# Kernel optimization log

Hardware: AMD Instinct MI355X
Metric: run time of the kernel (lower is better)

The kernel has to match this reference:

```python
import jax, jax.numpy as jnp
import numpy as np

N_NODES = 50000
N_EDGES = 800000
D_IN = 64
D_OUT = 64


def setup_inputs() -> dict:
    key = jax.random.key(0)
    k1, k2, k3, k4 = jax.random.split(key, 4)
    x = jax.random.normal(k1, (N_NODES, D_IN), dtype=jnp.float32)
    W = jax.random.normal(k2, (D_IN, D_OUT), dtype=jnp.float32) / np.sqrt(D_IN)
    bias = jnp.zeros((D_OUT,), dtype=jnp.float32)
    # learned per-edge weights (AdaptiveEdgeWeightGNN.edge_attr, initialized from fixed_values)
    edge_weight = jax.random.uniform(k3, (N_EDGES,), dtype=jnp.float32)
    edge_index = jax.random.randint(k4, (2, N_EDGES), 0, N_NODES, dtype=jnp.int64)
    return {"x": x, "W": W, "bias": bias, "edge_weight": edge_weight, "edge_index": edge_index}


def reference(x, W, bias, edge_weight, edge_index):
    # PyG GCNConv forward: gcn_norm (add self-loops, symmetric normalization
    # using the edge weights), linear transform, gather-scale-scatter, + bias.
    N = x.shape[0]
    row = edge_index[0]  # source nodes
    col = edge_index[1]  # target nodes
    loop = jnp.arange(N, dtype=edge_index.dtype)
    row = jnp.concatenate([row, loop])
    col = jnp.concatenate([col, loop])
    ew = jnp.concatenate([edge_weight, jnp.ones((N,), dtype=edge_weight.dtype)])
    # degree from edge weights scattered onto target nodes
    deg = jax.ops.segment_sum(ew, col, num_segments=N)
    deg_inv_sqrt = jnp.where(deg > 0, jax.lax.rsqrt(deg), 0.0)
    norm = deg_inv_sqrt[row] * ew * deg_inv_sqrt[col]  # [E+N]
    xw = x @ W  # [N, D_OUT]
    msgs = xw[row] * norm[:, None]  # gather + scale
    out = jax.ops.segment_sum(msgs, col, num_segments=N)  # scatter-add
    return out + bias
```

## Files before the change

kernel.cpp:

```cpp
#include <hip/hip_runtime.h>

#define N_NODES 50000
#define N_EDGES 800000
#define D 64
#define NCHUNK 64
#define CHUNK_E (N_EDGES / NCHUNK)
#define NRANGE 4
#define RANGE_N 16384
#define NB_NODE 196
#define PLACE_BLOCKS (N_EDGES / 256)
#define FLAGBIT 0x80000000u

typedef int iv4 __attribute__((ext_vector_type(4)));

__device__ __forceinline__ unsigned short f2bf(float f) {
    unsigned int u = __float_as_uint(f);
    u += 0x7FFFu + ((u >> 16) & 1u);
    return (unsigned short)(u >> 16);
}
__device__ __forceinline__ float bf2f(unsigned int s) {
    return __uint_as_float(s << 16);
}

__global__ __launch_bounds__(1024) void k_hist(const int* __restrict__ col,
                                               unsigned short* __restrict__ part,
                                               unsigned short* __restrict__ lrank,
                                               unsigned int* __restrict__ partials) {
    __shared__ unsigned int h[RANGE_N / 2];
    int i = blockIdx.x >> 2;
    int j = blockIdx.x & 3;
    int t = threadIdx.x;
    if (blockIdx.x == 0 && t < 256) partials[t] = 0;
    for (int k = t; k < RANGE_N / 2; k += 1024) h[k] = 0;
    __syncthreads();
    int base = i * CHUNK_E;
    for (int e = base + t; e < base + CHUNK_E; e += 1024) {
        int c = col[e];
        if ((c >> 14) == j) {
            int local = c & (RANGE_N - 1);
            int sh = (local & 1) << 4;
            unsigned int lr = atomicAdd(&h[local >> 1], 1u << sh);
            lrank[e] = (unsigned short)((lr >> sh) & 0xffffu);
        }
    }
    __syncthreads();
    for (int k = t; k < RANGE_N; k += 1024) {
        int n = j * RANGE_N + k;
        if (n < N_NODES)
            part[(size_t)i * N_NODES + n] =
                (unsigned short)((h[k >> 1] >> ((k & 1) << 4)) & 0xffffu);
    }
}

__global__ __launch_bounds__(256) void k_scan(unsigned short* __restrict__ part,
                                              int* __restrict__ start,
                                              unsigned int* __restrict__ partials) {
    __shared__ int s[256];
    __shared__ int red[256];
    int b = blockIdx.x, t = threadIdx.x;
    int n = b * 256 + t;
    unsigned int run = 0;
    if (n < N_NODES) {
        unsigned int vals[NCHUNK];
#pragma unroll
        for (int i = 0; i < NCHUNK; ++i)
            vals[i] = part[(size_t)i * N_NODES + n];
#pragma unroll
        for (int i = 0; i < NCHUNK; ++i) {
            part[(size_t)i * N_NODES + n] = (unsigned short)run;
            run += vals[i];
        }
    }
    int cnt = (n < N_NODES) ? (int)run : 0;
    s[t] = cnt;
    __syncthreads();
    for (int off = 1; off < 256; off <<= 1) {
        int a = (t >= off) ? s[t - off] : 0;
        __syncthreads();
        s[t] += a;
        __syncthreads();
    }
    if (t == 255)
        __hip_atomic_store(&partials[b], (unsigned int)s[255] | FLAGBIT,
                           __ATOMIC_RELEASE, __HIP_MEMORY_SCOPE_AGENT);
    unsigned int pv = 0;
    if (t < b) {
        unsigned int v;
        do {
            v = __hip_atomic_load(&partials[t], __ATOMIC_ACQUIRE, __HIP_MEMORY_SCOPE_AGENT);
        } while (!(v & FLAGBIT));
        pv = v & ~FLAGBIT;
    }
    red[t] = (int)pv;
    __syncthreads();
    for (int off = 128; off > 0; off >>= 1) {
        if (t < off) red[t] += red[t + off];
        __syncthreads();
    }
    int offset = red[0];
    if (n <= N_NODES) start[n] = offset + s[t] - cnt;
}

__global__ __launch_bounds__(256) void k_place(const int* __restrict__ ei,
                                               const float* __restrict__ ew,
                                               const int* __restrict__ start,
                                               const unsigned short* __restrict__ part,
                                               const unsigned short* __restrict__ lrank,
                                               unsigned int* __restrict__ rec) {
    int e = blockIdx.x * 256 + threadIdx.x;
    int c = ei[N_EDGES + e];
    int i = e / CHUNK_E;
    int pos = start[c] + (int)part[(size_t)i * N_NODES + c] + (int)lrank[e];
    rec[pos] = (unsigned int)ei[e] | ((unsigned int)f2bf(ew[e]) << 16);
}

__global__ __launch_bounds__(256, 4) void k_xw(const float* __restrict__ x,
                                               const float* __restrict__ W,
                                               const int* __restrict__ start,
                                               const unsigned int* __restrict__ rec,
                                               float* __restrict__ dis,
                                               unsigned short* __restrict__ xw16) {
    __shared__ float Ws[64 * 64];
    __shared__ float dls[64];
    int t = threadIdx.x;
    int r0 = blockIdx.x * 64;
    for (int i = t; i < 1024; i += 256)
        ((float4*)Ws)[i] = ((const float4*)W)[i];

    {
        int q = t >> 2, l = t & 3;
        int node = r0 + q;
        float s = 0.f;
        if (node < N_NODES) {
            int j0 = start[node], j1 = start[node + 1];
            for (int j = j0 + l; j < j1; j += 4) s += bf2f(rec[j] >> 16);
        }
        s += __shfl_xor(s, 1);
        s += __shfl_xor(s, 2);
        if (l == 0 && node < N_NODES) {
            float dv = rsqrtf(1.0f + s);
            dls[q] = dv;
            dis[node] = dv;
        }
    }
    __syncthreads();

    int cg = t & 15;
    int rg = t >> 4;
    int ra = min(r0 + rg,      N_NODES - 1);
    int rb = min(r0 + rg + 16, N_NODES - 1);
    int rc = min(r0 + rg + 32, N_NODES - 1);
    int rd = min(r0 + rg + 48, N_NODES - 1);
    const float4* x4 = (const float4*)x;

    float4 acc0 = make_float4(0.f, 0.f, 0.f, 0.f);
    float4 acc1 = acc0, acc2 = acc0, acc3 = acc0;

#pragma unroll 1
    for (int k4 = 0; k4 < 16; ++k4) {
        float4 xv0 = x4[ra * 16 + k4];
        float4 xv1 = x4[rb * 16 + k4];
        float4 xv2 = x4[rc * 16 + k4];
        float4 xv3 = x4[rd * 16 + k4];
        float4 w0 = *(const float4*)&Ws[(k4 * 4 + 0) * 64 + cg * 4];
        float4 w1 = *(const float4*)&Ws[(k4 * 4 + 1) * 64 + cg * 4];
        float4 w2 = *(const float4*)&Ws[(k4 * 4 + 2) * 64 + cg * 4];
        float4 w3 = *(const float4*)&Ws[(k4 * 4 + 3) * 64 + cg * 4];
        acc0.x = fmaf(xv0.x, w0.x, acc0.x); acc0.y = fmaf(xv0.x, w0.y, acc0.y);
        acc0.z = fmaf(xv0.x, w0.z, acc0.z); acc0.w = fmaf(xv0.x, w0.w, acc0.w);
        acc0.x = fmaf(xv0.y, w1.x, acc0.x); acc0.y = fmaf(xv0.y, w1.y, acc0.y);
        acc0.z = fmaf(xv0.y, w1.z, acc0.z); acc0.w = fmaf(xv0.y, w1.w, acc0.w);
        acc0.x = fmaf(xv0.z, w2.x, acc0.x); acc0.y = fmaf(xv0.z, w2.y, acc0.y);
        acc0.z = fmaf(xv0.z, w2.z, acc0.z); acc0.w = fmaf(xv0.z, w2.w, acc0.w);
        acc0.x = fmaf(xv0.w, w3.x, acc0.x); acc0.y = fmaf(xv0.w, w3.y, acc0.y);
        acc0.z = fmaf(xv0.w, w3.z, acc0.z); acc0.w = fmaf(xv0.w, w3.w, acc0.w);
        acc1.x = fmaf(xv1.x, w0.x, acc1.x); acc1.y = fmaf(xv1.x, w0.y, acc1.y);
        acc1.z = fmaf(xv1.x, w0.z, acc1.z); acc1.w = fmaf(xv1.x, w0.w, acc1.w);
        acc1.x = fmaf(xv1.y, w1.x, acc1.x); acc1.y = fmaf(xv1.y, w1.y, acc1.y);
        acc1.z = fmaf(xv1.y, w1.z, acc1.z); acc1.w = fmaf(xv1.y, w1.w, acc1.w);
        acc1.x = fmaf(xv1.z, w2.x, acc1.x); acc1.y = fmaf(xv1.z, w2.y, acc1.y);
        acc1.z = fmaf(xv1.z, w2.z, acc1.z); acc1.w = fmaf(xv1.z, w2.w, acc1.w);
        acc1.x = fmaf(xv1.w, w3.x, acc1.x); acc1.y = fmaf(xv1.w, w3.y, acc1.y);
        acc1.z = fmaf(xv1.w, w3.z, acc1.z); acc1.w = fmaf(xv1.w, w3.w, acc1.w);
        acc2.x = fmaf(xv2.x, w0.x, acc2.x); acc2.y = fmaf(xv2.x, w0.y, acc2.y);
        acc2.z = fmaf(xv2.x, w0.z, acc2.z); acc2.w = fmaf(xv2.x, w0.w, acc2.w);
        acc2.x = fmaf(xv2.y, w1.x, acc2.x); acc2.y = fmaf(xv2.y, w1.y, acc2.y);
        acc2.z = fmaf(xv2.y, w1.z, acc2.z); acc2.w = fmaf(xv2.y, w1.w, acc2.w);
        acc2.x = fmaf(xv2.z, w2.x, acc2.x); acc2.y = fmaf(xv2.z, w2.y, acc2.y);
        acc2.z = fmaf(xv2.z, w2.z, acc2.z); acc2.w = fmaf(xv2.z, w2.w, acc2.w);
        acc2.x = fmaf(xv2.w, w3.x, acc2.x); acc2.y = fmaf(xv2.w, w3.y, acc2.y);
        acc2.z = fmaf(xv2.w, w3.z, acc2.z); acc2.w = fmaf(xv2.w, w3.w, acc2.w);
        acc3.x = fmaf(xv3.x, w0.x, acc3.x); acc3.y = fmaf(xv3.x, w0.y, acc3.y);
        acc3.z = fmaf(xv3.x, w0.z, acc3.z); acc3.w = fmaf(xv3.x, w0.w, acc3.w);
        acc3.x = fmaf(xv3.y, w1.x, acc3.x); acc3.y = fmaf(xv3.y, w1.y, acc3.y);
        acc3.z = fmaf(xv3.y, w1.z, acc3.z); acc3.w = fmaf(xv3.y, w1.w, acc3.w);
        acc3.x = fmaf(xv3.z, w2.x, acc3.x); acc3.y = fmaf(xv3.z, w2.y, acc3.y);
        acc3.z = fmaf(xv3.z, w2.z, acc3.z); acc3.w = fmaf(xv3.z, w2.w, acc3.w);
        acc3.x = fmaf(xv3.w, w3.x, acc3.x); acc3.y = fmaf(xv3.w, w3.y, acc3.y);
        acc3.z = fmaf(xv3.w, w3.z, acc3.z); acc3.w = fmaf(xv3.w, w3.w, acc3.w);
    }

    float4 accs[4] = { acc0, acc1, acc2, acc3 };
#pragma unroll
    for (int i = 0; i < 4; ++i) {
        int row = r0 + rg + 16 * i;
        if (row < N_NODES) {
            float s = dls[rg + 16 * i];
            ushort4 s4 = make_ushort4(f2bf(accs[i].x * s), f2bf(accs[i].y * s),
                                      f2bf(accs[i].z * s), f2bf(accs[i].w * s));
            *(ushort4*)&xw16[row * 64 + cg * 4] = s4;
        }
    }
}

__global__ __launch_bounds__(256) void k_gather(const int* __restrict__ start,
                                                const unsigned int* __restrict__ rec,
                                                const unsigned short* __restrict__ xw16,
                                                const float* __restrict__ dis,
                                                const float* __restrict__ bias,
                                                float* __restrict__ out) {
    int wave = threadIdx.x >> 6;
    int c = threadIdx.x & 63;
    int n = blockIdx.x * 4 + wave;
    float di = dis[n];
    float acc[8];
#pragma unroll
    for (int k = 0; k < 8; ++k) acc[k] = 0.f;
    acc[0] = bf2f((unsigned int)xw16[n * 64 + c]);
    int j0  = __builtin_amdgcn_readfirstlane(start[n]);
    int cnt = __builtin_amdgcn_readfirstlane(start[n + 1]) - j0;
    int nit = (cnt + 7) >> 3;
    const iv4* rq = (const iv4*)(rec + j0);
    for (int it = 0; it < nit; ++it) {
        iv4 qa = rq[2 * it], qb = rq[2 * it + 1];
        unsigned int r[8];
        r[0] = (unsigned int)__builtin_amdgcn_readfirstlane(qa.x);
        r[1] = (unsigned int)__builtin_amdgcn_readfirstlane(qa.y);
        r[2] = (unsigned int)__builtin_amdgcn_readfirstlane(qa.z);
        r[3] = (unsigned int)__builtin_amdgcn_readfirstlane(qa.w);
        r[4] = (unsigned int)__builtin_amdgcn_readfirstlane(qb.x);
        r[5] = (unsigned int)__builtin_amdgcn_readfirstlane(qb.y);
        r[6] = (unsigned int)__builtin_amdgcn_readfirstlane(qb.z);
        r[7] = (unsigned int)__builtin_amdgcn_readfirstlane(qb.w);
        float v[8];
#pragma unroll
        for (int k = 0; k < 8; ++k)
            v[k] = bf2f((unsigned int)xw16[(r[k] & 0xffffu) * 64 + c]);
        int rem = cnt - (it << 3);
#pragma unroll
        for (int k = 0; k < 8; ++k) {
            float w = (k < rem) ? bf2f(r[k] >> 16) : 0.0f;
            acc[k] = fmaf(v[k], w, acc[k]);
        }
    }
    float a = ((acc[0] + acc[1]) + (acc[2] + acc[3])) + ((acc[4] + acc[5]) + (acc[6] + acc[7]));
    out[n * 64 + c] = fmaf(a, di, bias[c]);
}

extern "C" void kernel_launch(void* const* d_in, const int* in_sizes, int n_in,
                              void* d_out, int out_size, void* d_ws, size_t ws_size,
                              hipStream_t stream) {
    const float* x    = (const float*)d_in[0];
    const float* W    = (const float*)d_in[1];
    const float* bias = (const float*)d_in[2];
    const float* ew   = (const float*)d_in[3];
    const int*   ei   = (const int*)d_in[4];
    float* out = (float*)d_out;

    char* wsb = (char*)d_ws;
    unsigned int*   rec   = (unsigned int*)wsb;
    unsigned short* xw16  = (unsigned short*)(wsb + 6200000);
    unsigned short* lrank = (unsigned short*)(wsb + 12600000);
    unsigned short* part  = (unsigned short*)(wsb + 14200000);
    float*          dis   = (float*)(wsb + 20600000);
    int*            start = (int*)(wsb + 21000000);
    unsigned int*   partials = (unsigned int*)(wsb + 21300000);

    k_hist<<<NCHUNK * NRANGE, 1024, 0, stream>>>(ei + N_EDGES, part, lrank, partials);
    k_scan<<<NB_NODE, 256, 0, stream>>>(part, start, partials);
    k_place<<<PLACE_BLOCKS, 256, 0, stream>>>(ei, ew, start, part, lrank, rec);
    k_xw<<<(N_NODES + 63) / 64, 256, 0, stream>>>(x, W, start, rec, dis, xw16);
    k_gather<<<N_NODES / 4, 256, 0, stream>>>(start, rec, xw16, dis, bias, out);
}
```

Baseline: 84.72 us.

## Split per-node chunk scan across four lanes and launch more scan blocks

The scan kernel now assigns each node to four threads. Each thread handles 16 of the 64 chunk counts, and the four threads combine their sums with a sub-wavefront shuffle scan. Each block covers 64 nodes, so 782 blocks are launched instead of 196. This exposes more memory-level parallelism and occupancy on a kernel that was latency bound with few blocks and 64 serial loads per thread. The trade-off is more blocks in the decoupled-lookback chain: each block now sums up to 781 predecessor flags in a strided loop, which adds spin-wait and global atomic traffic. The partials array is also cleared over 1024 entries.

Result: slower. 157.9 us (+86.4%).

```diff
diff --git a/kernel.cpp b/kernel.cpp
--- a/kernel.cpp
+++ b/kernel.cpp
@@ -7,7 +7,7 @@
 #define CHUNK_E (N_EDGES / NCHUNK)
 #define NRANGE 4
 #define RANGE_N 16384
-#define NB_NODE 196
+#define SCAN_BLOCKS 782
 #define PLACE_BLOCKS (N_EDGES / 256)
 #define FLAGBIT 0x80000000u
 
@@ -30,7 +30,7 @@
     int i = blockIdx.x >> 2;
     int j = blockIdx.x & 3;
     int t = threadIdx.x;
-    if (blockIdx.x == 0 && t < 256) partials[t] = 0;
+    if (blockIdx.x == 0 && t < 1024) partials[t] = 0;
     for (int k = t; k < RANGE_N / 2; k += 1024) h[k] = 0;
     __syncthreads();
     int base = i * CHUNK_E;
@@ -52,53 +52,66 @@
     }
 }
 
-__global__ __launch_bounds__(256) void k_scan(unsigned short* __restrict__ part,
-                                              int* __restrict__ start,
-                                              unsigned int* __restrict__ partials) {
-    __shared__ int s[256];
-    __shared__ int red[256];
+__global__ __launch_bounds__(256, 6) void k_scan(unsigned short* __restrict__ part,
+                                                 int* __restrict__ start,
+                                                 unsigned int* __restrict__ partials) {
+    __shared__ int snode[64];
+    __shared__ int sred[256];
     int b = blockIdx.x, t = threadIdx.x;
-    int n = b * 256 + t;
-    unsigned int run = 0;
+    int q = t >> 2, l = t & 3;
+    int n = b * 64 + q;
+    unsigned int vals[16];
+    unsigned int lsum = 0;
     if (n < N_NODES) {
-        unsigned int vals[NCHUNK];
-#pragma unroll
-        for (int i = 0; i < NCHUNK; ++i)
-            vals[i] = part[(size_t)i * N_NODES + n];
-#pragma unroll
-        for (int i = 0; i < NCHUNK; ++i) {
-            part[(size_t)i * N_NODES + n] = (unsigned short)run;
+#pragma unroll
+        for (int i = 0; i < 16; ++i) {
+            vals[i] = part[(size_t)(l * 16 + i) * N_NODES + n];
+            lsum += vals[i];
+        }
+    }
+    unsigned int x = lsum;
+    unsigned int y = __shfl_up(x, 1, 4); if (l >= 1) x += y;
+    y = __shfl_up(x, 2, 4); if (l >= 2) x += y;
+    unsigned int excl = x - lsum;
+    unsigned int cnt = __shfl(x, 3, 4);
+    if (n < N_NODES) {
+        unsigned int run = excl;
+#pragma unroll
+        for (int i = 0; i < 16; ++i) {
+            part[(size_t)(l * 16 + i) * N_NODES + n] = (unsigned short)run;
             run += vals[i];
         }
     }
-    int cnt = (n < N_NODES) ? (int)run : 0;
-    s[t] = cnt;
-    __syncthreads();
-    for (int off = 1; off < 256; off <<= 1) {
-        int a = (t >= off) ? s[t - off] : 0;
-        __syncthreads();
-        s[t] += a;
-        __syncthreads();
-    }
-    if (t == 255)
-        __hip_atomic_store(&partials[b], (unsigned int)s[255] | FLAGBIT,
-                           __ATOMIC_RELEASE, __HIP_MEMORY_SCOPE_AGENT);
-    unsigned int pv = 0;
-    if (t < b) {
+    if (l == 0) snode[q] = (n < N_NODES) ? (int)cnt : 0;
+    __syncthreads();
+    if (t < 64) {
+        int v = snode[t];
+        int ix = v;
+        for (int off = 1; off < 64; off <<= 1) {
+            int u = __shfl_up(ix, off, 64);
+            if (t >= off) ix += u;
+        }
+        snode[t] = ix - v;
+        if (t == 63)
+            __hip_atomic_store(&partials[b], (unsigned int)ix | FLAGBIT,
+                               __ATOMIC_RELEASE, __HIP_MEMORY_SCOPE_AGENT);
+    }
+    int psum = 0;
+    for (int t2 = t; t2 < b; t2 += 256) {
         unsigned int v;
         do {
-            v = __hip_atomic_load(&partials[t], __ATOMIC_ACQUIRE, __HIP_MEMORY_SCOPE_AGENT);
+            v = __hip_atomic_load(&partials[t2], __ATOMIC_ACQUIRE, __HIP_MEMORY_SCOPE_AGENT);
         } while (!(v & FLAGBIT));
-        pv = v & ~FLAGBIT;
-    }
-    red[t] = (int)pv;
+        psum += (int)(v & ~FLAGBIT);
+    }
+    sred[t] = psum;
     __syncthreads();
     for (int off = 128; off > 0; off >>= 1) {
-        if (t < off) red[t] += red[t + off];
+        if (t < off) sred[t] += sred[t + off];
         __syncthreads();
     }
-    int offset = red[0];
-    if (n <= N_NODES) start[n] = offset + s[t] - cnt;
+    int offset = sred[0];
+    if (l == 0 && n <= N_NODES) start[n] = offset + snode[q];
 }
 
 __global__ __launch_bounds__(256) void k_place(const int* __restrict__ ei,
@@ -277,7 +290,7 @@
     unsigned int*   partials = (unsigned int*)(wsb + 21300000);
 
     k_hist<<<NCHUNK * NRANGE, 1024, 0, stream>>>(ei + N_EDGES, part, lrank, partials);
-    k_scan<<<NB_NODE, 256, 0, stream>>>(part, start, partials);
+    k_scan<<<SCAN_BLOCKS, 256, 0, stream>>>(part, start, partials);
     k_place<<<PLACE_BLOCKS, 256, 0, stream>>>(ei, ew, start, part, lrank, rec);
     k_xw<<<(N_NODES + 63) / 64, 256, 0, stream>>>(x, W, start, rec, dis, xw16);
     k_gather<<<N_NODES / 4, 256, 0, stream>>>(start, rec, xw16, dis, bias, out);
```

## Split node scan into three kernels and parallelize per-node chunk scan across four lanes

Applied to the files above, without the earlier changes.

Replaces the single scan kernel, which had each thread serially read and rewrite 64 chunk counts and used a decoupled look-back spin on flagged partials, with three kernels. The first spreads each node's 64 chunk counts over 4 lanes with a shuffle scan across 782 blocks for more memory parallelism. The second does the block-local scan and writes partials, and the third adds the cross-block prefix. This removes the spin-wait and raises occupancy, at the cost of two extra kernel launches and an extra pass over start.

Result: faster. 82.03 us (median of 2 runs) (-3.2%).

```diff
diff --git a/kernel.cpp b/kernel.cpp
--- a/kernel.cpp
+++ b/kernel.cpp
@@ -7,9 +7,9 @@
 #define CHUNK_E (N_EDGES / NCHUNK)
 #define NRANGE 4
 #define RANGE_N 16384
+#define SCANA_BLOCKS 782
 #define NB_NODE 196
 #define PLACE_BLOCKS (N_EDGES / 256)
-#define FLAGBIT 0x80000000u
 
 typedef int iv4 __attribute__((ext_vector_type(4)));
 
@@ -24,13 +24,11 @@
 
 __global__ __launch_bounds__(1024) void k_hist(const int* __restrict__ col,
                                                unsigned short* __restrict__ part,
-                                               unsigned short* __restrict__ lrank,
-                                               unsigned int* __restrict__ partials) {
+                                               unsigned short* __restrict__ lrank) {
     __shared__ unsigned int h[RANGE_N / 2];
     int i = blockIdx.x >> 2;
     int j = blockIdx.x & 3;
     int t = threadIdx.x;
-    if (blockIdx.x == 0 && t < 256) partials[t] = 0;
     for (int k = t; k < RANGE_N / 2; k += 1024) h[k] = 0;
     __syncthreads();
     int base = i * CHUNK_E;
@@ -52,26 +50,39 @@
     }
 }
 
-__global__ __launch_bounds__(256) void k_scan(unsigned short* __restrict__ part,
-                                              int* __restrict__ start,
-                                              unsigned int* __restrict__ partials) {
+__global__ __launch_bounds__(256) void k_scanA(unsigned short* __restrict__ part,
+                                               int* __restrict__ nodecnt) {
+    int b = blockIdx.x, t = threadIdx.x;
+    int q = t >> 2, l = t & 3;
+    int n = b * 64 + q;
+    if (n >= N_NODES) return;
+    unsigned int vals[16];
+    unsigned int lsum = 0;
+#pragma unroll
+    for (int i = 0; i < 16; ++i) {
+        vals[i] = part[(size_t)(l * 16 + i) * N_NODES + n];
+        lsum += vals[i];
+    }
+    unsigned int x = lsum;
+    unsigned int y = __shfl_up(x, 1, 4); if (l >= 1) x += y;
+    y = __shfl_up(x, 2, 4); if (l >= 2) x += y;
+    unsigned int excl = x - lsum;
+    unsigned int run = excl;
+#pragma unroll
+    for (int i = 0; i < 16; ++i) {
+        part[(size_t)(l * 16 + i) * N_NODES + n] = (unsigned short)run;
+        run += vals[i];
+    }
+    if (l == 3) nodecnt[n] = (int)x;
+}
+
+__global__ __launch_bounds__(256) void k_scanB(const int* __restrict__ nodecnt,
+                                               int* __restrict__ start,
+                                               int* __restrict__ partials) {
     __shared__ int s[256];
-    __shared__ int red[256];
     int b = blockIdx.x, t = threadIdx.x;
     int n = b * 256 + t;
-    unsigned int run = 0;
-    if (n < N_NODES) {
-        unsigned int vals[NCHUNK];
-#pragma unroll
-        for (int i = 0; i < NCHUNK; ++i)
-            vals[i] = part[(size_t)i * N_NODES + n];
-#pragma unroll
-        for (int i = 0; i < NCHUNK; ++i) {
-            part[(size_t)i * N_NODES + n] = (unsigned short)run;
-            run += vals[i];
-        }
-    }
-    int cnt = (n < N_NODES) ? (int)run : 0;
+    int cnt = (n < N_NODES) ? nodecnt[n] : 0;
     s[t] = cnt;
     __syncthreads();
     for (int off = 1; off < 256; off <<= 1) {
@@ -80,25 +91,23 @@
         s[t] += a;
         __syncthreads();
     }
-    if (t == 255)
-        __hip_atomic_store(&partials[b], (unsigned int)s[255] | FLAGBIT,
-                           __ATOMIC_RELEASE, __HIP_MEMORY_SCOPE_AGENT);
-    unsigned int pv = 0;
-    if (t < b) {
-        unsigned int v;
-        do {
-            v = __hip_atomic_load(&partials[t], __ATOMIC_ACQUIRE, __HIP_MEMORY_SCOPE_AGENT);
-        } while (!(v & FLAGBIT));
-        pv = v & ~FLAGBIT;
-    }
-    red[t] = (int)pv;
+    if (n <= N_NODES) start[n] = s[t] - cnt;
+    if (t == 255) partials[b] = s[255];
+}
+
+__global__ __launch_bounds__(256) void k_scanC(int* __restrict__ start,
+                                               const int* __restrict__ partials) {
+    __shared__ int red[256];
+    int b = blockIdx.x, t = threadIdx.x;
+    red[t] = (t < b) ? partials[t] : 0;
     __syncthreads();
     for (int off = 128; off > 0; off >>= 1) {
         if (t < off) red[t] += red[t + off];
         __syncthreads();
     }
     int offset = red[0];
-    if (n <= N_NODES) start[n] = offset + s[t] - cnt;
+    int n = b * 256 + t;
+    if (n <= N_NODES) start[n] += offset;
 }
 
 __global__ __launch_bounds__(256) void k_place(const int* __restrict__ ei,
@@ -274,10 +283,13 @@
     unsigned short* part  = (unsigned short*)(wsb + 14200000);
     float*          dis   = (float*)(wsb + 20600000);
     int*            start = (int*)(wsb + 21000000);
-    unsigned int*   partials = (unsigned int*)(wsb + 21300000);
-
-    k_hist<<<NCHUNK * NRANGE, 1024, 0, stream>>>(ei + N_EDGES, part, lrank, partials);
-    k_scan<<<NB_NODE, 256, 0, stream>>>(part, start, partials);
+    int*            nodecnt = (int*)(wsb + 21300000);
+    int*            partials = (int*)(wsb + 21600000);
+
+    k_hist<<<NCHUNK * NRANGE, 1024, 0, stream>>>(ei + N_EDGES, part, lrank);
+    k_scanA<<<SCANA_BLOCKS, 256, 0, stream>>>(part, nodecnt);
+    k_scanB<<<NB_NODE, 256, 0, stream>>>(nodecnt, start, partials);
+    k_scanC<<<NB_NODE, 256, 0, stream>>>(start, partials);
     k_place<<<PLACE_BLOCKS, 256, 0, stream>>>(ei, ew, start, part, lrank, rec);
     k_xw<<<(N_NODES + 63) / 64, 256, 0, stream>>>(x, W, start, rec, dis, xw16);
     k_gather<<<N_NODES / 4, 256, 0, stream>>>(start, rec, xw16, dis, bias, out);
```
